# Performance work log

Measured on AMD Instinct MI355X. Metric: run time of the kernel, lower is better.

Reference implementation:

```python
import jax, jax.numpy as jnp
import numpy as np

D_MODEL = 2048
N_HEADS = 16
HEAD_DIM = D_MODEL // N_HEADS
SEGMENT_SIZE = 512
DILATION = 2
BATCH = 2
SEQ_LEN = 8192


def setup_inputs() -> dict:
    key = jax.random.key(0)
    k1, k2, k3 = jax.random.split(key, 3)
    x = jax.random.normal(k1, (BATCH, SEQ_LEN, D_MODEL), dtype=jnp.float32)
    Wqkv = jax.random.normal(k2, (3 * D_MODEL, D_MODEL), dtype=jnp.float32) * 0.02
    b_qkv = jnp.zeros((3 * D_MODEL,), dtype=jnp.float32)
    Wout = jax.random.normal(k3, (D_MODEL, D_MODEL), dtype=jnp.float32) * 0.02
    b_out = jnp.zeros((D_MODEL,), dtype=jnp.float32)
    return {"x": x, "Wqkv": Wqkv, "b_qkv": b_qkv, "Wout": Wout, "b_out": b_out}


def reference(x, Wqkv, b_qkv, Wout, b_out):
    B, S, D = x.shape
    H, hd = N_HEADS, HEAD_DIM
    # dilated segment gather: [B, n_seg, seg, D] strided by dilation -> [B, n_seg, L, D]
    xs = x.reshape(B, -1, SEGMENT_SIZE, D)[:, :, ::DILATION, :]
    N, L = xs.shape[1], xs.shape[2]
    # fused qkv projection (FlashMHA.Wqkv)
    qkv = jnp.einsum('bnld,ed->bnle', xs, Wqkv) + b_qkv  # [B,N,L,3D]
    q, k, v = jnp.split(qkv, 3, axis=-1)
    q = q.reshape(B, N, L, H, hd)
    k = k.reshape(B, N, L, H, hd)
    v = v.reshape(B, N, L, H, hd)
    scale = 1.0 / jnp.sqrt(jnp.asarray(hd, dtype=x.dtype))
    # per-segment attention over the dilated tokens
    scores = jnp.einsum('bnqhd,bnkhd->bnhqk', q, k) * scale  # [B,N,H,L,L]
    attn = jax.nn.softmax(scores, axis=-1)
    out = jnp.einsum('bnhqk,bnkhd->bnqhd', attn, v).reshape(B, N, L, D)
    # output projection (FlashMHA.out_proj)
    out = jnp.einsum('bnld,ed->bnle', out, Wout) + b_out
    # merge segments back: [B, N*L, D]
    return out.reshape(B, -1, D)
```

## Files before the change

kernel.cpp:

```cpp
#include <hip/hip_runtime.h>
#include <hip/hip_bf16.h>
#include <stdint.h>

#define DEVI __device__ __forceinline__

typedef __attribute__((ext_vector_type(8))) short bf16x8;
typedef __attribute__((ext_vector_type(4))) float f32x4;


DEVI unsigned short f2bf(float f) {
  unsigned int u = __float_as_uint(f);
  return (unsigned short)((u + 0x7fffu + ((u >> 16) & 1u)) >> 16);
}

DEVI void load_lds16(const void* g, void* l) {
  __builtin_amdgcn_global_load_lds(
      (const __attribute__((address_space(1))) unsigned int*)g,
      (__attribute__((address_space(3))) unsigned int*)l, 16, 0, 0);
}

DEVI bf16x8 ld8(const unsigned short* p) {
  return *reinterpret_cast<const bf16x8*>(p);
}

__global__ void k_gather(const float* __restrict__ x, unsigned short* __restrict__ xs) {
  int i = blockIdx.x * 256 + threadIdx.x;
  int r = i >> 9;
  int c = (i & 511) << 2;
  int b = r >> 12;
  int rem = r & 4095;
  int seg = rem >> 8;
  int lcl = rem & 255;
  long src_row = (long)b * 8192 + seg * 512 + lcl * 2;
  const float4 v = *reinterpret_cast<const float4*>(x + src_row * 2048 + c);
  uint2 o;
  o.x = f2bf(v.x) | ((unsigned)f2bf(v.y) << 16);
  o.y = f2bf(v.z) | ((unsigned)f2bf(v.w) << 16);
  *reinterpret_cast<uint2*>(xs + (long)r * 2048 + c) = o;
}

__global__ void k_cast(const float* __restrict__ in, unsigned short* __restrict__ out, int n4) {
  int i = blockIdx.x * 256 + threadIdx.x;
  if (i >= n4) return;
  const float4 v = *reinterpret_cast<const float4*>(in + (long)i * 4);
  uint2 o;
  o.x = f2bf(v.x) | ((unsigned)f2bf(v.y) << 16);
  o.y = f2bf(v.z) | ((unsigned)f2bf(v.w) << 16);
  *reinterpret_cast<uint2*>(out + (long)i * 4) = o;
}


DEVI unsigned short* lds_of(unsigned short* smem, int tile, int op) {
  return smem + (tile & 3) * 16384 + op * 8192;
}

DEVI void stage_op(const unsigned short* gb, int K, int kt,
                   unsigned short* region, int t, int w) {
#pragma unroll
  for (int i = 0; i < 2; ++i) {
    int s = i * 512 + t;
    int prow = s >> 3;
    int cs = s & 7;
    int c = cs ^ (prow & 7);
    int r = prow * 2 + (c >> 2);
    int k0 = (c & 3) << 3;
    load_lds16(gb + (long)r * K + kt * 32 + k0,
               (char*)region + i * 8192 + w * 1024);
  }
}

#define FRAG_A(dst, mm)                                                      \
  { int r_ = wm * 128 + (mm) * 16 + lr;                                      \
    int p_ = r_ >> 1;                                                        \
    int cs_ = (((r_ & 1) << 2) | lq) ^ (p_ & 7);                             \
    dst = ld8(Ab_ + p_ * 64 + cs_ * 8); }
#define FRAG_B(dst, nn)                                                      \
  { int r_ = wn * 64 + (nn) * 16 + lr;                                       \
    int p_ = r_ >> 1;                                                        \
    int cs_ = (((r_ & 1) << 2) | lq) ^ (p_ & 7);                             \
    dst = ld8(Bb_ + p_ * 64 + cs_ * 8); }
#define MM(mm, areg)                                                         \
  acc[mm][0] = __builtin_amdgcn_mfma_f32_16x16x32_bf16(areg, bf0, acc[mm][0], 0, 0, 0); \
  acc[mm][1] = __builtin_amdgcn_mfma_f32_16x16x32_bf16(areg, bf1, acc[mm][1], 0, 0, 0); \
  acc[mm][2] = __builtin_amdgcn_mfma_f32_16x16x32_bf16(areg, bf2, acc[mm][2], 0, 0, 0); \
  acc[mm][3] = __builtin_amdgcn_mfma_f32_16x16x32_bf16(areg, bf3, acc[mm][3], 0, 0, 0);

#define TILE(JEXPR, VMTRAIL, DOSTAGE)                                        \
  {                                                                          \
    const int j_ = (JEXPR);                                                  \
    const unsigned short* Ab_ = smem + (j_ & 3) * 16384;                     \
    const unsigned short* Bb_ = Ab_ + 8192;                                  \
    bf16x8 af0, af1, af2, af3, bf0, bf1, bf2, bf3;                           \
                             \
    FRAG_B(bf0, 0) FRAG_B(bf1, 1) FRAG_B(bf2, 2) FRAG_B(bf3, 3)              \
    FRAG_A(af0, 0) FRAG_A(af1, 1) FRAG_A(af2, 2) FRAG_A(af3, 3)              \
    if (DOSTAGE) stage_op(Agb, K, j_ + 3, lds_of(smem, j_ + 3, 0), t, w);    \
    __builtin_amdgcn_s_barrier();                                            \
    asm volatile("s_waitcnt lgkmcnt(0)" ::: "memory");                       \
    __builtin_amdgcn_sched_barrier(0);                                       \
    __builtin_amdgcn_s_setprio(1);                                           \
    MM(0, af0) MM(1, af1) MM(2, af2) MM(3, af3)                              \
    __builtin_amdgcn_s_setprio(0);                                           \
    __builtin_amdgcn_s_barrier();                                            \
    __builtin_amdgcn_sched_barrier(0);                                       \
                             \
    FRAG_A(af0, 4) FRAG_A(af1, 5) FRAG_A(af2, 6) FRAG_A(af3, 7)              \
    if (DOSTAGE) stage_op(Bgb, K, j_ + 3, lds_of(smem, j_ + 3, 1), t, w);    \
    __builtin_amdgcn_s_barrier();                                            \
    asm volatile("s_waitcnt lgkmcnt(0)" ::: "memory");                       \
    __builtin_amdgcn_sched_barrier(0);                                       \
    __builtin_amdgcn_s_setprio(1);                                           \
    MM(4, af0) MM(5, af1) MM(6, af2) MM(7, af3)                              \
    __builtin_amdgcn_s_setprio(0);                                           \
    asm volatile("s_waitcnt vmcnt(" VMTRAIL ")" ::: "memory");               \
    __builtin_amdgcn_s_barrier();                                            \
    __builtin_amdgcn_sched_barrier(0);                                       \
  }

template <bool BF16_OUT>
__global__ __launch_bounds__(512, 1)
void k_gemm(const unsigned short* __restrict__ A, const unsigned short* __restrict__ B,
            const float* __restrict__ bias, void* __restrict__ Cv, int N, int K) {
  __shared__ unsigned short smem[65536];
  const int nbx = N >> 8;
  const int cpx = gridDim.x >> 3;
  const int id = blockIdx.x;
  const int sw = (id & 7) * cpx + (id >> 3);
  const int bx = sw % nbx, by = sw / nbx;
  const int t = threadIdx.x, w = t >> 6, l = t & 63;
  const int lr = l & 15, lq = l >> 4;
  const int wm = w >> 2, wn = w & 3;
  const unsigned short* Agb = A + (long)by * 256 * K;
  const unsigned short* Bgb = B + (long)bx * 256 * K;
  const int nk = K >> 5;
  f32x4 acc[8][4] = {};

  for (int jt = 0; jt < 3; ++jt) {
    stage_op(Agb, K, jt, lds_of(smem, jt, 0), t, w);
    stage_op(Bgb, K, jt, lds_of(smem, jt, 1), t, w);
  }
  asm volatile("s_waitcnt vmcnt(8)" ::: "memory");
  __builtin_amdgcn_s_barrier();

  for (int j = 0; j < nk - 3; ++j) TILE(j, "8", true)
  TILE(nk - 3, "4", false)
  TILE(nk - 2, "0", false)
  TILE(nk - 1, "0", false)

  const long crow0 = (long)by * 256 + wm * 128;
  const int ccol0 = bx * 256 + wn * 64;
#pragma unroll
  for (int n = 0; n < 4; ++n) {
    int col = ccol0 + n * 16 + lr;
    float bv = bias[col];
#pragma unroll
    for (int m = 0; m < 8; ++m) {
      long r0 = crow0 + m * 16 + lq * 4;
#pragma unroll
      for (int r = 0; r < 4; ++r) {
        float v = acc[m][n][r] + bv;
        if (BF16_OUT)
          ((unsigned short*)Cv)[(r0 + r) * N + col] = f2bf(v);
        else
          ((float*)Cv)[(r0 + r) * N + col] = v;
      }
    }
  }
}

__global__ __launch_bounds__(512)
void k_attn(const unsigned short* __restrict__ qkv, unsigned short* __restrict__ aout) {
  __shared__ unsigned short smem[65536];
  unsigned short* Kl = smem;
  unsigned short* Vt = smem + 32768;
  const int p = blockIdx.x;
  const int h = p & 15;
  const long rb = (long)(p >> 4) * 256;
  const int t = threadIdx.x, w = t >> 6, l = t & 63;
  const int lr = l & 15, lq = l >> 4;

  const unsigned short* kb = qkv + rb * 6144 + 2048 + h * 128;
#pragma unroll
  for (int i = 0; i < 8; ++i) {
    int s = i * 512 + t;
    int row = s >> 4;
    int ch = (s & 15) ^ (row & 7);
    load_lds16(kb + (long)row * 6144 + ch * 8, (char*)Kl + i * 8192 + w * 1024);
  }
  const unsigned short* vb = qkv + rb * 6144 + 4096 + h * 128;
#pragma unroll
  for (int j0 = 0; j0 < 8; ++j0) {
    int k = j0 * 32 + (t >> 4);
    int d0 = (t & 15) * 8;
    bf16x8 v = ld8(vb + (long)k * 6144 + d0);
#pragma unroll
    for (int j = 0; j < 8; ++j) {
      int d = d0 + j;
      int ch = (k >> 3) ^ ((d ^ (d >> 3)) & 7);
      Vt[d * 256 + ch * 8 + (k & 7)] = (unsigned short)(short)v[j];
    }
  }
  const unsigned short* qb = qkv + (rb + w * 32) * 6144 + h * 128;
  bf16x8 qa[2][4];
#pragma unroll
  for (int m = 0; m < 2; ++m)
#pragma unroll
    for (int kt = 0; kt < 4; ++kt)
      qa[m][kt] = ld8(qb + (long)(m * 16 + lr) * 6144 + kt * 32 + lq * 8);

  __syncthreads();

  f32x4 sacc[2][16] = {};
#pragma unroll
  for (int n = 0; n < 16; ++n) {
    int row = n * 16 + lr;
#pragma unroll
    for (int kt = 0; kt < 4; ++kt) {
      int ch = (kt * 4 + lq) ^ (row & 7);
      bf16x8 kf = ld8(Kl + row * 128 + ch * 8);
      sacc[0][n] = __builtin_amdgcn_mfma_f32_16x16x32_bf16(qa[0][kt], kf, sacc[0][n], 0, 0, 0);
      sacc[1][n] = __builtin_amdgcn_mfma_f32_16x16x32_bf16(qa[1][kt], kf, sacc[1][n], 0, 0, 0);
    }
  }
  const float scale = 0.08838834764831845f;
  float mx[2][4], sm[2][4];
#pragma unroll
  for (int m = 0; m < 2; ++m)
#pragma unroll
    for (int r = 0; r < 4; ++r) {
      float v = sacc[m][0][r];
#pragma unroll
      for (int n = 1; n < 16; ++n) v = fmaxf(v, sacc[m][n][r]);
      mx[m][r] = v;
      sm[m][r] = 0.f;
    }
#pragma unroll
  for (int mk = 1; mk < 16; mk <<= 1)
#pragma unroll
    for (int m = 0; m < 2; ++m)
#pragma unroll
      for (int r = 0; r < 4; ++r)
        mx[m][r] = fmaxf(mx[m][r], __shfl_xor(mx[m][r], mk));
#pragma unroll
  for (int m = 0; m < 2; ++m)
#pragma unroll
    for (int n = 0; n < 16; ++n)
#pragma unroll
      for (int r = 0; r < 4; ++r) {
        float e = __expf((sacc[m][n][r] - mx[m][r]) * scale);
        sacc[m][n][r] = e;
        sm[m][r] += e;
      }
#pragma unroll
  for (int mk = 1; mk < 16; mk <<= 1)
#pragma unroll
    for (int m = 0; m < 2; ++m)
#pragma unroll
      for (int r = 0; r < 4; ++r)
        sm[m][r] += __shfl_xor(sm[m][r], mk);
  float ri[2][4];
#pragma unroll
  for (int m = 0; m < 2; ++m)
#pragma unroll
    for (int r = 0; r < 4; ++r) ri[m][r] = 1.0f / sm[m][r];

  unsigned int pb[2][16][2];
#pragma unroll
  for (int m = 0; m < 2; ++m)
#pragma unroll
    for (int n = 0; n < 16; ++n) {
      pb[m][n][0] = f2bf(sacc[m][n][0] * ri[m][0]) | ((unsigned)f2bf(sacc[m][n][1] * ri[m][1]) << 16);
      pb[m][n][1] = f2bf(sacc[m][n][2] * ri[m][2]) | ((unsigned)f2bf(sacc[m][n][3] * ri[m][3]) << 16);
    }

  __syncthreads();
  unsigned short* Pl = Kl + w * 4096;
  f32x4 oacc[2][8] = {};
#pragma unroll
  for (int half = 0; half < 2; ++half) {
#pragma unroll
    for (int m = 0; m < 2; ++m)
#pragma unroll
      for (int n = 0; n < 8; ++n) {
        int col = n * 16 + lr;
        int row0 = m * 16 + lq * 4;
#pragma unroll
        for (int pr = 0; pr < 2; ++pr) {
          unsigned int u = pb[m][half * 8 + n][pr];
          int ra = row0 + pr * 2, rbw = ra + 1;
          int ca = (col >> 3) ^ (ra & 7);
          int cb = (col >> 3) ^ (rbw & 7);
          Pl[ra * 128 + ca * 8 + (col & 7)] = (unsigned short)(u & 0xffffu);
          Pl[rbw * 128 + cb * 8 + (col & 7)] = (unsigned short)(u >> 16);
        }
      }
#pragma unroll
    for (int kt = 0; kt < 4; ++kt) {
      bf16x8 pa[2];
#pragma unroll
      for (int m = 0; m < 2; ++m) {
        int row = m * 16 + lr;
        int ch = (kt * 4 + lq) ^ (row & 7);
        pa[m] = ld8(Pl + row * 128 + ch * 8);
      }
#pragma unroll
      for (int dt = 0; dt < 8; ++dt) {
        int d = dt * 16 + lr;
        int kg = half * 128 + kt * 32 + lq * 8;
        int ch = (kg >> 3) ^ ((d ^ (d >> 3)) & 7);
        bf16x8 vf = ld8(Vt + d * 256 + ch * 8);
        oacc[0][dt] = __builtin_amdgcn_mfma_f32_16x16x32_bf16(pa[0], vf, oacc[0][dt], 0, 0, 0);
        oacc[1][dt] = __builtin_amdgcn_mfma_f32_16x16x32_bf16(pa[1], vf, oacc[1][dt], 0, 0, 0);
      }
    }
  }
  unsigned short* ob = aout + (rb + w * 32) * 2048 + h * 128;
#pragma unroll
  for (int m = 0; m < 2; ++m)
#pragma unroll
    for (int dt = 0; dt < 8; ++dt)
#pragma unroll
      for (int r = 0; r < 4; ++r)
        ob[(long)(m * 16 + lq * 4 + r) * 2048 + dt * 16 + lr] = f2bf(oacc[m][dt][r]);
}

extern "C" void kernel_launch(void* const* d_in, const int* in_sizes, int n_in,
                              void* d_out, int out_size, void* d_ws, size_t ws_size,
                              hipStream_t stream) {
  const float* x     = (const float*)d_in[0];
  const float* Wqkv  = (const float*)d_in[1];
  const float* b_qkv = (const float*)d_in[2];
  const float* Wout  = (const float*)d_in[3];
  const float* b_out = (const float*)d_in[4];
  float* out = (float*)d_out;

  char* ws = (char*)d_ws;
  unsigned short* xs   = (unsigned short*)(ws);
  unsigned short* aout = xs;
  unsigned short* wq   = (unsigned short*)(ws + 33554432);
  unsigned short* wo   = (unsigned short*)(ws + 58720256);
  unsigned short* qkv  = (unsigned short*)(ws + 67108864);

  k_gather<<<16384, 256, 0, stream>>>(x, xs);
  k_cast<<<12288, 256, 0, stream>>>(Wqkv, wq, 3145728);
  k_cast<<<4096, 256, 0, stream>>>(Wout, wo, 1048576);
  k_gemm<true><<<32 * 24, 512, 0, stream>>>(xs, wq, b_qkv, (void*)qkv, 6144, 2048);
  k_attn<<<512, 512, 0, stream>>>(qkv, aout);
  k_gemm<false><<<32 * 8, 512, 0, stream>>>(aout, wo, b_out, (void*)out, 2048, 2048);
}
```

Measured before the change: 367.2 us.

## Switch GEMM to BK=64 double-buffered LDS pipeline with new swizzle

Restructures the bf16 MFMA GEMM mainloop from a 4-deep ring of 32-wide K tiles to a 2-deep double buffer of 64-wide K tiles. All global-to-LDS loads for the next tile are issued at the start of each iteration, and each iteration now has four MFMA phases instead of two. The LDS layout and XOR swizzle change to one 64-element row per tile row. This halves the number of loop iterations and the barrier and waitcnt overhead per unit of K. The cost is shallower prefetch (one tile ahead instead of three) and a full vmcnt(0) drain every iteration, which could expose global memory latency.

```diff
diff --git a/kernel.cpp b/kernel.cpp
--- a/kernel.cpp
+++ b/kernel.cpp
@@ -50,71 +50,78 @@
 }
 
 
-DEVI unsigned short* lds_of(unsigned short* smem, int tile, int op) {
-  return smem + (tile & 3) * 16384 + op * 8192;
-}
-
-DEVI void stage_op(const unsigned short* gb, int K, int kt,
-                   unsigned short* region, int t, int w) {
+DEVI void stage_piece(const unsigned short* gb, int K, int kt, int h,
+                      unsigned short* opbuf, int t, int w) {
 #pragma unroll
   for (int i = 0; i < 2; ++i) {
     int s = i * 512 + t;
-    int prow = s >> 3;
+    int lrow = s >> 3;
     int cs = s & 7;
-    int c = cs ^ (prow & 7);
-    int r = prow * 2 + (c >> 2);
-    int k0 = (c & 3) << 3;
-    load_lds16(gb + (long)r * K + kt * 32 + k0,
-               (char*)region + i * 8192 + w * 1024);
-  }
-}
-
-#define FRAG_A(dst, mm)                                                      \
+    int c = cs ^ (lrow & 7);
+    load_lds16(gb + (long)(h * 128 + lrow) * K + kt * 64 + c * 8,
+               (char*)opbuf + h * 16384 + i * 8192 + w * 1024);
+  }
+}
+
+#define FRAG_A(dst, mm, kk)                                                  \
   { int r_ = wm * 128 + (mm) * 16 + lr;                                      \
-    int p_ = r_ >> 1;                                                        \
-    int cs_ = (((r_ & 1) << 2) | lq) ^ (p_ & 7);                             \
-    dst = ld8(Ab_ + p_ * 64 + cs_ * 8); }
-#define FRAG_B(dst, nn)                                                      \
+    int ch_ = ((kk) * 4 + lq) ^ (r_ & 7);                                    \
+    dst = ld8(Ab_ + r_ * 64 + ch_ * 8); }
+#define FRAG_B(dst, nn, kk)                                                  \
   { int r_ = wn * 64 + (nn) * 16 + lr;                                       \
-    int p_ = r_ >> 1;                                                        \
-    int cs_ = (((r_ & 1) << 2) | lq) ^ (p_ & 7);                             \
-    dst = ld8(Bb_ + p_ * 64 + cs_ * 8); }
+    int ch_ = ((kk) * 4 + lq) ^ (r_ & 7);                                    \
+    dst = ld8(Bb_ + r_ * 64 + ch_ * 8); }
 #define MM(mm, areg)                                                         \
   acc[mm][0] = __builtin_amdgcn_mfma_f32_16x16x32_bf16(areg, bf0, acc[mm][0], 0, 0, 0); \
   acc[mm][1] = __builtin_amdgcn_mfma_f32_16x16x32_bf16(areg, bf1, acc[mm][1], 0, 0, 0); \
   acc[mm][2] = __builtin_amdgcn_mfma_f32_16x16x32_bf16(areg, bf2, acc[mm][2], 0, 0, 0); \
   acc[mm][3] = __builtin_amdgcn_mfma_f32_16x16x32_bf16(areg, bf3, acc[mm][3], 0, 0, 0);
 
-#define TILE(JEXPR, VMTRAIL, DOSTAGE)                                        \
-  {                                                                          \
-    const int j_ = (JEXPR);                                                  \
-    const unsigned short* Ab_ = smem + (j_ & 3) * 16384;                     \
-    const unsigned short* Bb_ = Ab_ + 8192;                                  \
-    bf16x8 af0, af1, af2, af3, bf0, bf1, bf2, bf3;                           \
-                             \
-    FRAG_B(bf0, 0) FRAG_B(bf1, 1) FRAG_B(bf2, 2) FRAG_B(bf3, 3)              \
-    FRAG_A(af0, 0) FRAG_A(af1, 1) FRAG_A(af2, 2) FRAG_A(af3, 3)              \
-    if (DOSTAGE) stage_op(Agb, K, j_ + 3, lds_of(smem, j_ + 3, 0), t, w);    \
+#define PHASE_MM(m0, m1, m2, m3)                                             \
     __builtin_amdgcn_s_barrier();                                            \
     asm volatile("s_waitcnt lgkmcnt(0)" ::: "memory");                       \
     __builtin_amdgcn_sched_barrier(0);                                       \
     __builtin_amdgcn_s_setprio(1);                                           \
-    MM(0, af0) MM(1, af1) MM(2, af2) MM(3, af3)                              \
+    MM(m0, af0) MM(m1, af1) MM(m2, af2) MM(m3, af3)                          \
     __builtin_amdgcn_s_setprio(0);                                           \
     __builtin_amdgcn_s_barrier();                                            \
-    __builtin_amdgcn_sched_barrier(0);                                       \
-                             \
-    FRAG_A(af0, 4) FRAG_A(af1, 5) FRAG_A(af2, 6) FRAG_A(af3, 7)              \
-    if (DOSTAGE) stage_op(Bgb, K, j_ + 3, lds_of(smem, j_ + 3, 1), t, w);    \
+    asm volatile("" ::: "memory");
+
+#define PHASE_MM_LAST(m0, m1, m2, m3)                                        \
     __builtin_amdgcn_s_barrier();                                            \
     asm volatile("s_waitcnt lgkmcnt(0)" ::: "memory");                       \
     __builtin_amdgcn_sched_barrier(0);                                       \
     __builtin_amdgcn_s_setprio(1);                                           \
-    MM(4, af0) MM(5, af1) MM(6, af2) MM(7, af3)                              \
+    MM(m0, af0) MM(m1, af1) MM(m2, af2) MM(m3, af3)                          \
     __builtin_amdgcn_s_setprio(0);                                           \
-    asm volatile("s_waitcnt vmcnt(" VMTRAIL ")" ::: "memory");               \
+    asm volatile("s_waitcnt vmcnt(0)" ::: "memory");                         \
     __builtin_amdgcn_s_barrier();                                            \
-    __builtin_amdgcn_sched_barrier(0);                                       \
+    asm volatile("" ::: "memory");
+
+#define TILE64(JEXPR, DOSTAGE)                                               \
+  {                                                                          \
+    const int j_ = (JEXPR);                                                  \
+    const unsigned short* Ab_ = smem + (j_ & 1) * 32768;                     \
+    const unsigned short* Bb_ = Ab_ + 16384;                                 \
+    unsigned short* An_ = smem + ((j_ + 1) & 1) * 32768;                     \
+    unsigned short* Bn_ = An_ + 16384;                                       \
+    if (DOSTAGE) {                                                           \
+      stage_piece(Agb, K, j_ + 1, 0, An_, t, w);                             \
+      stage_piece(Bgb, K, j_ + 1, 0, Bn_, t, w);                             \
+      stage_piece(Agb, K, j_ + 1, 1, An_, t, w);                             \
+      stage_piece(Bgb, K, j_ + 1, 1, Bn_, t, w);                             \
+    }                                                                        \
+    bf16x8 af0, af1, af2, af3, bf0, bf1, bf2, bf3;                           \
+    FRAG_B(bf0, 0, 0) FRAG_B(bf1, 1, 0) FRAG_B(bf2, 2, 0) FRAG_B(bf3, 3, 0)  \
+    FRAG_A(af0, 0, 0) FRAG_A(af1, 1, 0) FRAG_A(af2, 2, 0) FRAG_A(af3, 3, 0)  \
+    PHASE_MM(0, 1, 2, 3)                                                     \
+    FRAG_A(af0, 4, 0) FRAG_A(af1, 5, 0) FRAG_A(af2, 6, 0) FRAG_A(af3, 7, 0)  \
+    PHASE_MM(4, 5, 6, 7)                                                     \
+    FRAG_B(bf0, 0, 1) FRAG_B(bf1, 1, 1) FRAG_B(bf2, 2, 1) FRAG_B(bf3, 3, 1)  \
+    FRAG_A(af0, 0, 1) FRAG_A(af1, 1, 1) FRAG_A(af2, 2, 1) FRAG_A(af3, 3, 1)  \
+    PHASE_MM(0, 1, 2, 3)                                                     \
+    FRAG_A(af0, 4, 1) FRAG_A(af1, 5, 1) FRAG_A(af2, 6, 1) FRAG_A(af3, 7, 1)  \
+    PHASE_MM_LAST(4, 5, 6, 7)                                                \
   }
 
 template <bool BF16_OUT>
@@ -132,20 +139,19 @@
   const int wm = w >> 2, wn = w & 3;
   const unsigned short* Agb = A + (long)by * 256 * K;
   const unsigned short* Bgb = B + (long)bx * 256 * K;
-  const int nk = K >> 5;
+  const int nk = K >> 6;
   f32x4 acc[8][4] = {};
 
-  for (int jt = 0; jt < 3; ++jt) {
-    stage_op(Agb, K, jt, lds_of(smem, jt, 0), t, w);
-    stage_op(Bgb, K, jt, lds_of(smem, jt, 1), t, w);
-  }
-  asm volatile("s_waitcnt vmcnt(8)" ::: "memory");
+  stage_piece(Agb, K, 0, 0, smem, t, w);
+  stage_piece(Bgb, K, 0, 0, smem + 16384, t, w);
+  stage_piece(Agb, K, 0, 1, smem, t, w);
+  stage_piece(Bgb, K, 0, 1, smem + 16384, t, w);
+  asm volatile("s_waitcnt vmcnt(0)" ::: "memory");
   __builtin_amdgcn_s_barrier();
-
-  for (int j = 0; j < nk - 3; ++j) TILE(j, "8", true)
-  TILE(nk - 3, "4", false)
-  TILE(nk - 2, "0", false)
-  TILE(nk - 1, "0", false)
+  asm volatile("" ::: "memory");
+
+  for (int j = 0; j < nk - 1; ++j) TILE64(j, true)
+  TILE64(nk - 1, false)
 
   const long crow0 = (long)by * 256 + wm * 128;
   const int ccol0 = bx * 256 + wn * 64;
```

Measured after the change: 370.8 us. About the same (+1.0%).

## Shorten GEMM prefetch depth and stage epilogue through LDS for vector stores

Applied to the files above, without the earlier changes.

The GEMM main loop now prefetches two K-tiles ahead instead of three, using the same 4-slot LDS ring. It also drops a couple of scheduling barriers and adjusts the vmcnt waits to match. The epilogue no longer writes scalar 2- or 4-byte values scattered by MFMA lane layout. Each wave instead stages its 16x64 sub-tile in a padded LDS scratch area and reads it back as rows, so global writes become 16-byte coalesced stores. The shallower prefetch may expose more global-load latency in exchange.

```diff
diff --git a/kernel.cpp b/kernel.cpp
--- a/kernel.cpp
+++ b/kernel.cpp
@@ -50,22 +50,18 @@
 }
 
 
-DEVI unsigned short* lds_of(unsigned short* smem, int tile, int op) {
-  return smem + (tile & 3) * 16384 + op * 8192;
-}
-
-DEVI void stage_op(const unsigned short* gb, int K, int kt,
-                   unsigned short* region, int t, int w) {
+DEVI void stage_piece(const unsigned short* gb, int K, int h, int op,
+                      unsigned short* smem, int t, int w) {
+  char* base = (char*)(smem + (h & 3) * 16384 + op * 8192);
 #pragma unroll
   for (int i = 0; i < 2; ++i) {
     int s = i * 512 + t;
     int prow = s >> 3;
-    int cs = s & 7;
-    int c = cs ^ (prow & 7);
-    int r = prow * 2 + (c >> 2);
-    int k0 = (c & 3) << 3;
-    load_lds16(gb + (long)r * K + kt * 32 + k0,
-               (char*)region + i * 8192 + w * 1024);
+    int cs8 = s & 7;
+    int c8 = cs8 ^ (prow & 7);
+    int r = prow * 2 + (c8 >> 2);
+    int k0 = (c8 & 3) << 3;
+    load_lds16(gb + (long)r * K + h * 32 + k0, base + i * 8192 + w * 1024);
   }
 }
 
@@ -85,16 +81,15 @@
   acc[mm][2] = __builtin_amdgcn_mfma_f32_16x16x32_bf16(areg, bf2, acc[mm][2], 0, 0, 0); \
   acc[mm][3] = __builtin_amdgcn_mfma_f32_16x16x32_bf16(areg, bf3, acc[mm][3], 0, 0, 0);
 
-#define TILE(JEXPR, VMTRAIL, DOSTAGE)                                        \
+#define HALF(HEXPR, DOSTAGE, VMLIT)                                          \
   {                                                                          \
-    const int j_ = (JEXPR);                                                  \
-    const unsigned short* Ab_ = smem + (j_ & 3) * 16384;                     \
+    const int h_ = (HEXPR);                                                  \
+    const unsigned short* Ab_ = smem + (h_ & 3) * 16384;                     \
     const unsigned short* Bb_ = Ab_ + 8192;                                  \
     bf16x8 af0, af1, af2, af3, bf0, bf1, bf2, bf3;                           \
-                             \
     FRAG_B(bf0, 0) FRAG_B(bf1, 1) FRAG_B(bf2, 2) FRAG_B(bf3, 3)              \
     FRAG_A(af0, 0) FRAG_A(af1, 1) FRAG_A(af2, 2) FRAG_A(af3, 3)              \
-    if (DOSTAGE) stage_op(Agb, K, j_ + 3, lds_of(smem, j_ + 3, 0), t, w);    \
+    if (DOSTAGE) stage_piece(Agb, K, h_ + 2, 0, smem, t, w);                 \
     __builtin_amdgcn_s_barrier();                                            \
     asm volatile("s_waitcnt lgkmcnt(0)" ::: "memory");                       \
     __builtin_amdgcn_sched_barrier(0);                                       \
@@ -102,19 +97,16 @@
     MM(0, af0) MM(1, af1) MM(2, af2) MM(3, af3)                              \
     __builtin_amdgcn_s_setprio(0);                                           \
     __builtin_amdgcn_s_barrier();                                            \
-    __builtin_amdgcn_sched_barrier(0);                                       \
-                             \
     FRAG_A(af0, 4) FRAG_A(af1, 5) FRAG_A(af2, 6) FRAG_A(af3, 7)              \
-    if (DOSTAGE) stage_op(Bgb, K, j_ + 3, lds_of(smem, j_ + 3, 1), t, w);    \
+    if (DOSTAGE) stage_piece(Bgb, K, h_ + 2, 1, smem, t, w);                 \
     __builtin_amdgcn_s_barrier();                                            \
     asm volatile("s_waitcnt lgkmcnt(0)" ::: "memory");                       \
     __builtin_amdgcn_sched_barrier(0);                                       \
     __builtin_amdgcn_s_setprio(1);                                           \
     MM(4, af0) MM(5, af1) MM(6, af2) MM(7, af3)                              \
     __builtin_amdgcn_s_setprio(0);                                           \
-    asm volatile("s_waitcnt vmcnt(" VMTRAIL ")" ::: "memory");               \
+    asm volatile("s_waitcnt vmcnt(" VMLIT ")" ::: "memory");                 \
     __builtin_amdgcn_s_barrier();                                            \
-    __builtin_amdgcn_sched_barrier(0);                                       \
   }
 
 template <bool BF16_OUT>
@@ -132,37 +124,60 @@
   const int wm = w >> 2, wn = w & 3;
   const unsigned short* Agb = A + (long)by * 256 * K;
   const unsigned short* Bgb = B + (long)bx * 256 * K;
-  const int nk = K >> 5;
+  const int nh = K >> 5;
   f32x4 acc[8][4] = {};
 
-  for (int jt = 0; jt < 3; ++jt) {
-    stage_op(Agb, K, jt, lds_of(smem, jt, 0), t, w);
-    stage_op(Bgb, K, jt, lds_of(smem, jt, 1), t, w);
-  }
-  asm volatile("s_waitcnt vmcnt(8)" ::: "memory");
+  stage_piece(Agb, K, 0, 0, smem, t, w);
+  stage_piece(Bgb, K, 0, 1, smem, t, w);
+  stage_piece(Agb, K, 1, 0, smem, t, w);
+  stage_piece(Bgb, K, 1, 1, smem, t, w);
+  asm volatile("s_waitcnt vmcnt(4)" ::: "memory");
   __builtin_amdgcn_s_barrier();
 
-  for (int j = 0; j < nk - 3; ++j) TILE(j, "8", true)
-  TILE(nk - 3, "4", false)
-  TILE(nk - 2, "0", false)
-  TILE(nk - 1, "0", false)
+  for (int h = 0; h < nh - 2; ++h) HALF(h, true, "4")
+  HALF(nh - 2, false, "0")
+  HALF(nh - 1, false, "0")
 
   const long crow0 = (long)by * 256 + wm * 128;
   const int ccol0 = bx * 256 + wn * 64;
-#pragma unroll
-  for (int n = 0; n < 4; ++n) {
-    int col = ccol0 + n * 16 + lr;
-    float bv = bias[col];
+  float bv[4];
+#pragma unroll
+  for (int n = 0; n < 4; ++n) bv[n] = bias[ccol0 + n * 16 + lr];
+  const int lrr = l >> 2;
+  if (BF16_OUT) {
+    unsigned short* Lw = smem + w * 1216;
+    const int lcb = (l & 3) * 8;
 #pragma unroll
     for (int m = 0; m < 8; ++m) {
-      long r0 = crow0 + m * 16 + lq * 4;
-#pragma unroll
-      for (int r = 0; r < 4; ++r) {
-        float v = acc[m][n][r] + bv;
-        if (BF16_OUT)
-          ((unsigned short*)Cv)[(r0 + r) * N + col] = f2bf(v);
-        else
-          ((float*)Cv)[(r0 + r) * N + col] = v;
+#pragma unroll
+      for (int n = 0; n < 4; ++n)
+#pragma unroll
+        for (int r = 0; r < 4; ++r)
+          Lw[(lq * 4 + r) * 76 + n * 16 + lr] = f2bf(acc[m][n][r] + bv[n]);
+      asm volatile("s_waitcnt lgkmcnt(0)" ::: "memory");
+#pragma unroll
+      for (int rd = 0; rd < 2; ++rd) {
+        bf16x8 v = ld8(Lw + lrr * 76 + lcb + rd * 32);
+        *reinterpret_cast<bf16x8*>((unsigned short*)Cv +
+            (crow0 + m * 16 + lrr) * N + ccol0 + lcb + rd * 32) = v;
+      }
+    }
+  } else {
+    float* Lf = (float*)smem + w * 1216;
+    const int lcf = (l & 3) * 4;
+#pragma unroll
+    for (int m = 0; m < 8; ++m) {
+#pragma unroll
+      for (int n = 0; n < 4; ++n)
+#pragma unroll
+        for (int r = 0; r < 4; ++r)
+          Lf[(lq * 4 + r) * 76 + n * 16 + lr] = acc[m][n][r] + bv[n];
+      asm volatile("s_waitcnt lgkmcnt(0)" ::: "memory");
+#pragma unroll
+      for (int rd = 0; rd < 4; ++rd) {
+        float4 v = *reinterpret_cast<const float4*>(Lf + lrr * 76 + lcf + rd * 16);
+        *reinterpret_cast<float4*>((float*)Cv +
+            (crow0 + m * 16 + lrr) * N + ccol0 + lcf + rd * 16) = v;
       }
     }
   }
```

After: 354.3 us. 3.5% less time.
